# Optimization experiments

Measured on AMD Instinct MI355X. Metric: run time of the kernel, lower is better.

## Reference

```python
import jax, jax.numpy as jnp
import numpy as np

P, S, IMG = 8, 4, 256          # patch_size, stride, img_size
HID, GH, B = 64, 128, 4        # conv hidden ch, gcn hidden ch, batch
Ph = (IMG - P) // S + 1        # 63 patches per side
N = Ph * Ph                    # 3969 patch-nodes


def _conv(x, w, b):
    y = jax.lax.conv_general_dilated(x, w, (1, 1), 'SAME',
                                     dimension_numbers=('NCHW', 'OIHW', 'NCHW'))
    return y + b[None, :, None, None]


def _img2patch(x):
    # x: [B,1,H,W] -> [B, N, P*P] (row-major patch pixels, matching torch reshape)
    pt = jax.lax.conv_general_dilated_patches(x, (P, P), (S, S), 'VALID')  # [B, P*P, Ph, Pw]
    b = x.shape[0]
    return pt.reshape(b, P * P, N).transpose(0, 2, 1)


def _patch2img(y):
    # y: [b, N, P*P] -> [b, 1, IMG, IMG] via overlap scatter-add
    b = y.shape[0]
    y = y.reshape(b, Ph, Ph, P, P)
    x = jnp.zeros((b, 1, IMG, IMG), y.dtype)
    hi = S * (Ph - 1) + 1
    for i in range(P):          # fixed small loop over patch pixels (64 iters)
        for j in range(P):
            x = x.at[:, 0, i:i + hi:S, j:j + hi:S].add(y[:, :, :, i, j])
    return x


def _gcn(x, adj, w, bias):
    # x: [B,N,F_in], adj: [B,N,N] -> [B,N,F_out]
    support = jnp.einsum('bnf,fg->bng', x, w)
    return jnp.einsum('bnm,bmg->bng', adj, support) + bias


def setup_inputs() -> dict:
    key = jax.random.key(0)
    ks = jax.random.split(key, 14)
    sc = 0.05
    return {
        'input_data': jax.random.normal(ks[0], (B, 1, IMG, IMG), jnp.float32),
        'proj': jax.random.normal(ks[1], (B, 1, IMG, IMG), jnp.float32),
        'adj': jax.random.uniform(ks[2], (B, N, N), jnp.float32) / N,
        'lam': jnp.float32(0.5),
        'conv_w1': jax.random.normal(ks[3], (HID, 1, 3, 3), jnp.float32) * sc,
        'conv_b1': jnp.zeros((HID,), jnp.float32),
        'conv_w2': jax.random.normal(ks[4], (HID, HID, 3, 3), jnp.float32) * sc,
        'conv_b2': jnp.zeros((HID,), jnp.float32),
        'conv_w3': jax.random.normal(ks[5], (1, HID, 3, 3), jnp.float32) * sc,
        'conv_b3': jnp.zeros((1,), jnp.float32),
        'gcn_w3': jax.random.normal(ks[6], (P * P, GH), jnp.float32) * sc,
        'gcn_b3': jnp.zeros((GH,), jnp.float32),
        'gcn_w4': jax.random.normal(ks[7], (GH, P * P), jnp.float32) * sc,
        'gcn_b4': jnp.zeros((P * P,), jnp.float32),
    }


def reference(input_data, proj, adj, lam,
              conv_w1, conv_b1, conv_w2, conv_b2, conv_w3, conv_b3,
              gcn_w3, gcn_b3, gcn_w4, gcn_b4):
    # block1: data-fidelity step (fidelity_module modeled as DC update)
    tmp1 = input_data + lam * (proj - input_data)
    # block2: 3-layer CNN
    h = jax.nn.relu(_conv(input_data, conv_w1, conv_b1))
    h = jax.nn.relu(_conv(h, conv_w2, conv_b2))
    tmp2 = _conv(h, conv_w3, conv_b3)
    # block3/4: patch-graph GCN branch
    patch = _img2patch(input_data)                 # [B, N, P*P]
    g = jax.nn.relu(_gcn(patch, adj, gcn_w3, gcn_b3))
    g = _gcn(g, adj, gcn_w4, gcn_b4)               # [B, N, P*P]
    # Patch2Im with overlap-count normalization mask
    mask = _patch2img(jnp.ones((1, N, P * P), jnp.float32))
    tmp3 = _patch2img(g) / mask
    return jax.nn.relu(tmp1 + tmp2 + tmp3)
```

## Files before the change

### kernel.cpp

```cpp
#include <hip/hip_runtime.h>

#define IMG   256
#define NPIX  65536
#define PH    63
#define NNODE 3969
#define SN    4000
#define HID   64
#define GH    128
#define BATCH 4

typedef __attribute__((ext_vector_type(8))) short short8;
typedef __attribute__((ext_vector_type(4))) float float4v;
typedef unsigned short ushort_t;

__device__ inline ushort_t f2bf(float f) {
    union { float f; unsigned u; } v; v.f = f;
    unsigned r = v.u + 0x7FFF + ((v.u >> 16) & 1);
    return (ushort_t)(r >> 16);
}

__global__ __launch_bounds__(256) void k_cvt_adj(const float* __restrict__ adj,
                                                 ushort_t* __restrict__ adjb) {
    int n = blockIdx.x, b = blockIdx.y;
    const float* src = adj + (size_t)(b * NNODE + n) * NNODE;
    unsigned* dst = (unsigned*)(adjb + (size_t)(b * NNODE + n) * SN);
    for (int c2 = threadIdx.x; c2 < SN / 2; c2 += 256) {
        int c = c2 * 2;
        float f0 = (c < NNODE) ? src[c] : 0.f;
        float f1 = (c + 1 < NNODE) ? src[c + 1] : 0.f;
        dst[c2] = (unsigned)f2bf(f0) | ((unsigned)f2bf(f1) << 16);
    }
}

__global__ __launch_bounds__(256) void k_sup1(const float* __restrict__ in,
                                              const float* __restrict__ w3,
                                              ushort_t* __restrict__ sup1T) {
    int b = blockIdx.z;
    int g = blockIdx.y * 8 + (threadIdx.x >> 5);
    int n = blockIdx.x * 32 + (threadIdx.x & 31);
    ushort_t* dst = sup1T + (size_t)b * GH * SN + (size_t)g * SN + n;
    if (n >= NNODE) { *dst = 0; return; }
    int py = n / PH, px = n - py * PH;
    const float* base = in + (size_t)b * NPIX + (py * 4) * IMG + px * 4;
    float acc = 0.f;
#pragma unroll
    for (int i = 0; i < 8; ++i)
#pragma unroll
        for (int j = 0; j < 8; ++j)
            acc += base[i * IMG + j] * w3[(i * 8 + j) * GH + g];
    *dst = f2bf(acc);
}

template <int G>
__global__ __launch_bounds__(256) void k_gemm_mfma(const ushort_t* __restrict__ adjb,
                                                   const ushort_t* __restrict__ supT,
                                                   float* __restrict__ C) {
    constexpr int FN = (G == 128) ? 4 : 2;
    const int b = blockIdx.z, ks = blockIdx.y;
    const int node0 = blockIdx.x * 128;
    const int t = threadIdx.x;
    const int lane = t & 63, w = t >> 6;
    const int l15 = lane & 15, q = lane >> 4;
    const int wm0 = (G == 128) ? (w & 1) * 64 : 0;
    const int wn0 = (G == 128) ? (w >> 1) * 64 : w * 32;

    __shared__ ushort_t Als[G][72];
    __shared__ ushort_t Bls[128][72];

    const int k0c = ks * 992;
    const int kend = (ks == 3) ? NNODE : k0c + 992;
    const int kiters = (kend - k0c + 31) >> 5;
    const int npairs = (kiters + 1) >> 1;

    const ushort_t* Ab = supT + (size_t)b * G * SN;
    const ushort_t* Bb = adjb + (size_t)b * NNODE * SN;
    float* Cb = C + (size_t)b * G * SN;

    float4v acc[4][FN];
#pragma unroll
    for (int i = 0; i < 4; ++i)
#pragma unroll
        for (int j = 0; j < FN; ++j)
#pragma unroll
            for (int r = 0; r < 4; ++r) acc[i][j][r] = 0.f;

    for (int kp = 0; kp < npairs; ++kp) {
        const int kb0 = k0c + kp * 64;
        const bool has2 = (kp * 2 + 1 < kiters);
#pragma unroll
        for (int i = 0; i < G / 64; ++i) {
            int idx = t + i * 256;
            int r = idx >> 2, s = idx & 3;
            *(uint4*)&Als[r][s * 8] =
                *(const uint4*)&Ab[(size_t)r * SN + kb0 + s * 8];
        }
#pragma unroll
        for (int i = 0; i < 2; ++i) {
            int idx = t + i * 256;
            int r = idx >> 2, s = idx & 3;
            *(uint4*)&Bls[r][s * 8] =
                *(const uint4*)&Bb[(size_t)(node0 + r) * SN + kb0 + s * 8];
        }
        if (has2) {
#pragma unroll
            for (int i = 0; i < G / 64; ++i) {
                int idx = t + i * 256;
                int r = idx >> 2, s = idx & 3;
                *(uint4*)&Als[r][32 + s * 8] =
                    *(const uint4*)&Ab[(size_t)r * SN + kb0 + 32 + s * 8];
            }
#pragma unroll
            for (int i = 0; i < 2; ++i) {
                int idx = t + i * 256;
                int r = idx >> 2, s = idx & 3;
                *(uint4*)&Bls[r][32 + s * 8] =
                    *(const uint4*)&Bb[(size_t)(node0 + r) * SN + kb0 + 32 + s * 8];
            }
        }
        __syncthreads();
        {
            short8 af[4], bf[FN];
#pragma unroll
            for (int i = 0; i < 4; ++i)
                af[i] = *(const short8*)&Als[wm0 + i * 16 + l15][q * 8];
#pragma unroll
            for (int j = 0; j < FN; ++j)
                bf[j] = *(const short8*)&Bls[wn0 + j * 16 + l15][q * 8];
#pragma unroll
            for (int i = 0; i < 4; ++i)
#pragma unroll
                for (int j = 0; j < FN; ++j)
                    acc[i][j] = __builtin_amdgcn_mfma_f32_16x16x32_bf16(
                        af[i], bf[j], acc[i][j], 0, 0, 0);
        }
        if (has2) {
            short8 af[4], bf[FN];
#pragma unroll
            for (int i = 0; i < 4; ++i)
                af[i] = *(const short8*)&Als[wm0 + i * 16 + l15][32 + q * 8];
#pragma unroll
            for (int j = 0; j < FN; ++j)
                bf[j] = *(const short8*)&Bls[wn0 + j * 16 + l15][32 + q * 8];
#pragma unroll
            for (int i = 0; i < 4; ++i)
#pragma unroll
                for (int j = 0; j < FN; ++j)
                    acc[i][j] = __builtin_amdgcn_mfma_f32_16x16x32_bf16(
                        af[i], bf[j], acc[i][j], 0, 0, 0);
        }
        __syncthreads();
    }
#pragma unroll
    for (int i = 0; i < 4; ++i) {
        int gg = wm0 + i * 16 + q * 4;
#pragma unroll
        for (int j = 0; j < FN; ++j) {
            int nn = node0 + wn0 + j * 16 + l15;
            if (nn < NNODE) {
#pragma unroll
                for (int r = 0; r < 4; ++r)
                    unsafeAtomicAdd(&Cb[(size_t)(gg + r) * SN + nn], acc[i][j][r]);
            }
        }
    }
}

__global__ __launch_bounds__(256) void k_sup2(const float* __restrict__ g1T,
                                              const float* __restrict__ gb3,
                                              const float* __restrict__ w4,
                                              ushort_t* __restrict__ sup2T) {
    int b = blockIdx.z;
    int g = blockIdx.y * 8 + (threadIdx.x >> 5);
    int n = blockIdx.x * 32 + (threadIdx.x & 31);
    const float* gb = g1T + (size_t)b * GH * SN + n;
    float acc = 0.f;
#pragma unroll 8
    for (int k = 0; k < GH; ++k) {
        float v = fmaxf(gb[(size_t)k * SN] + gb3[k], 0.f);
        acc += v * w4[k * 64 + g];
    }
    sup2T[(size_t)b * 64 * SN + (size_t)g * SN + n] = (n < NNODE) ? f2bf(acc) : 0;
}

__global__ __launch_bounds__(256) void k_conv1(const float* __restrict__ in,
                                               const float* __restrict__ w,
                                               const float* __restrict__ bias,
                                               ushort_t* __restrict__ h1n) {
    int b = blockIdx.z;
    const float* inb = in + (size_t)b * NPIX;
    __shared__ float s[18][18];
    __shared__ float ws[576];
    int tx = threadIdx.x & 15, ty = threadIdx.x >> 4;
    int x0 = blockIdx.x * 16, y0 = blockIdx.y * 16;
    for (int idx = threadIdx.x; idx < 324; idx += 256) {
        int yy = idx / 18, xx = idx - yy * 18;
        int gy = y0 + yy - 1, gx = x0 + xx - 1;
        s[yy][xx] = (gy >= 0 && gy < IMG && gx >= 0 && gx < IMG) ? inb[gy * IMG + gx] : 0.f;
    }
    for (int idx = threadIdx.x; idx < 576; idx += 256) ws[idx] = w[idx];
    __syncthreads();
    float r[9];
#pragma unroll
    for (int dy = 0; dy < 3; ++dy)
#pragma unroll
        for (int dx = 0; dx < 3; ++dx) r[dy * 3 + dx] = s[ty + dy][tx + dx];
    int outp = (y0 + ty) * IMG + x0 + tx;
    ushort_t* dst = h1n + ((size_t)b * NPIX + outp) * 64;
#pragma unroll
    for (int sgrp = 0; sgrp < 8; ++sgrp) {
        unsigned pk[4];
#pragma unroll
        for (int h = 0; h < 4; ++h) {
            int oc0 = sgrp * 8 + h * 2;
            float a0 = bias[oc0], a1 = bias[oc0 + 1];
#pragma unroll
            for (int k = 0; k < 9; ++k) {
                a0 += r[k] * ws[oc0 * 9 + k];
                a1 += r[k] * ws[(oc0 + 1) * 9 + k];
            }
            a0 = fmaxf(a0, 0.f); a1 = fmaxf(a1, 0.f);
            pk[h] = (unsigned)f2bf(a0) | ((unsigned)f2bf(a1) << 16);
        }
        *(uint4*)&dst[sgrp * 8] = *(uint4*)pk;
    }
}

__global__ __launch_bounds__(256) void k_prepack(const float* __restrict__ w,
                                                 ushort_t* __restrict__ W2p) {
    int idx = blockIdx.x * 256 + threadIdx.x;
    if (idx >= 36864) return;
    int tap = idx >> 12, rem = idx & 4095;
    int oc = rem >> 6, ic = rem & 63;
    W2p[idx] = f2bf(w[(oc * 64 + ic) * 9 + tap]);
}

__global__ __launch_bounds__(256) void k_conv2(const ushort_t* __restrict__ h1n,
                                               const ushort_t* __restrict__ W2p,
                                               const float* __restrict__ bias,
                                               float* __restrict__ h2) {
    __shared__ ushort_t Xs[340 * 72];
    const int b = blockIdx.z;
    const ushort_t* h1b = h1n + (size_t)b * NPIX * 64;
    float* h2b = h2 + (size_t)b * 64 * NPIX;
    const int t = threadIdx.x;
    const int lane = t & 63, w = t >> 6;
    const int l15 = lane & 15, q = lane >> 4;
    const int x0 = blockIdx.x * 32, y0 = blockIdx.y * 8;

    for (int idx = t; idx < 2720; idx += 256) {
        int hp = idx >> 3, s = idx & 7;
        int hy = hp / 34, hx = hp - hy * 34;
        int gy = y0 + hy - 1, gx = x0 + hx - 1;
        uint4 v = {0u, 0u, 0u, 0u};
        if (gy >= 0 && gy < IMG && gx >= 0 && gx < IMG)
            v = *(const uint4*)&h1b[((size_t)gy * IMG + gx) * 64 + s * 8];
        *(uint4*)&Xs[hp * 72 + s * 8] = v;
    }
    __syncthreads();

    const int wn0 = w * 64;
    int pbase[4];
#pragma unroll
    for (int j = 0; j < 4; ++j) {
        int p = wn0 + j * 16 + l15;
        pbase[j] = (p >> 5) * 34 + (p & 31);
    }

    float4v acc[4][4];
#pragma unroll
    for (int i = 0; i < 4; ++i)
#pragma unroll
        for (int j = 0; j < 4; ++j)
#pragma unroll
            for (int r = 0; r < 4; ++r) acc[i][j][r] = 0.f;

    for (int tap = 0; tap < 9; ++tap) {
        int ky = tap / 3, kx = tap - ky * 3;
        const ushort_t* wp = W2p + tap * 4096;
#pragma unroll
        for (int c = 0; c < 2; ++c) {
            short8 af[4], bf[4];
#pragma unroll
            for (int i = 0; i < 4; ++i)
                af[i] = *(const short8*)&wp[(i * 16 + l15) * 64 + c * 32 + q * 8];
#pragma unroll
            for (int j = 0; j < 4; ++j)
                bf[j] = *(const short8*)&Xs[(pbase[j] + ky * 34 + kx) * 72 + c * 32 + q * 8];
#pragma unroll
            for (int i = 0; i < 4; ++i)
#pragma unroll
                for (int j = 0; j < 4; ++j)
                    acc[i][j] = __builtin_amdgcn_mfma_f32_16x16x32_bf16(
                        af[i], bf[j], acc[i][j], 0, 0, 0);
        }
    }

#pragma unroll
    for (int i = 0; i < 4; ++i) {
#pragma unroll
        for (int j = 0; j < 4; ++j) {
            int p = wn0 + j * 16 + l15;
            int y = y0 + (p >> 5), x = x0 + (p & 31);
#pragma unroll
            for (int r = 0; r < 4; ++r) {
                int oc = i * 16 + q * 4 + r;
                h2b[(size_t)oc * NPIX + (size_t)y * IMG + x] =
                    fmaxf(acc[i][j][r] + bias[oc], 0.f);
            }
        }
    }
}

__global__ __launch_bounds__(256) void k_combine(const float* __restrict__ in,
                                                 const float* __restrict__ proj,
                                                 const float* __restrict__ lamp,
                                                 const float* __restrict__ h2,
                                                 const float* __restrict__ wc,
                                                 const float* __restrict__ bc,
                                                 const float* __restrict__ g2T,
                                                 const float* __restrict__ gb4,
                                                 float* __restrict__ out) {
    int b = blockIdx.z;
    const float* inb = in + (size_t)b * NPIX;
    const float* prb = proj + (size_t)b * NPIX;
    const float* h2b = h2 + (size_t)b * 64 * NPIX;
    const float* g2b = g2T + (size_t)b * 64 * SN;
    __shared__ float s[16][18][18];
    __shared__ float ws[144];
    int tx = threadIdx.x & 15, ty = threadIdx.x >> 4;
    int x0 = blockIdx.x * 16, y0 = blockIdx.y * 16;
    int y = y0 + ty, x = x0 + tx;

    float acc = bc[0];
    for (int icc = 0; icc < 4; ++icc) {
        for (int idx = threadIdx.x; idx < 16 * 324; idx += 256) {
            int ic = idx / 324, rem = idx - ic * 324;
            int yy = rem / 18, xx = rem - yy * 18;
            int gy = y0 + yy - 1, gx = x0 + xx - 1;
            s[ic][yy][xx] = (gy >= 0 && gy < IMG && gx >= 0 && gx < IMG)
                                ? h2b[(icc * 16 + ic) * NPIX + gy * IMG + gx]
                                : 0.f;
        }
        for (int idx = threadIdx.x; idx < 144; idx += 256) ws[idx] = wc[icc * 144 + idx];
        __syncthreads();
#pragma unroll 4
        for (int ic = 0; ic < 16; ++ic) {
#pragma unroll
            for (int ky = 0; ky < 3; ++ky)
#pragma unroll
                for (int kx = 0; kx < 3; ++kx)
                    acc += s[ic][ty + ky][tx + kx] * ws[ic * 9 + ky * 3 + kx];
        }
        __syncthreads();
    }

    float iv = inb[y * IMG + x], pv = prb[y * IMG + x];
    float tmp1 = iv + lamp[0] * (pv - iv);

    int pylo = (y >= 4) ? ((y - 4) >> 2) : 0;
    int pyhi = min(62, y >> 2);
    int pxlo = (x >= 4) ? ((x - 4) >> 2) : 0;
    int pxhi = min(62, x >> 2);
    float sum = 0.f;
    int cnt = 0;
    for (int py = pylo; py <= pyhi; ++py)
        for (int px = pxlo; px <= pxhi; ++px) {
            int pix = (y - 4 * py) * 8 + (x - 4 * px);
            sum += g2b[(size_t)pix * SN + (py * PH + px)] + gb4[pix];
            ++cnt;
        }
    float tmp3 = sum / (float)cnt;

    out[(size_t)b * NPIX + y * IMG + x] = fmaxf(tmp1 + acc + tmp3, 0.f);
}

extern "C" void kernel_launch(void* const* d_in, const int* in_sizes, int n_in,
                              void* d_out, int out_size, void* d_ws, size_t ws_size,
                              hipStream_t stream) {
    const float* input = (const float*)d_in[0];
    const float* proj  = (const float*)d_in[1];
    const float* adj   = (const float*)d_in[2];
    const float* lam   = (const float*)d_in[3];
    const float* cw1   = (const float*)d_in[4];
    const float* cb1   = (const float*)d_in[5];
    const float* cw2   = (const float*)d_in[6];
    const float* cb2   = (const float*)d_in[7];
    const float* cw3   = (const float*)d_in[8];
    const float* cb3   = (const float*)d_in[9];
    const float* gw3   = (const float*)d_in[10];
    const float* gb3   = (const float*)d_in[11];
    const float* gw4   = (const float*)d_in[12];
    const float* gb4   = (const float*)d_in[13];
    float* out = (float*)d_out;

    char* base = (char*)d_ws;
    float*    g2T   = (float*)base;
    char*     pool  = base + 4096000;
    ushort_t* adjb  = (ushort_t*)pool;
    ushort_t* sup1T = (ushort_t*)(pool + 127008000);
    float*    g1T   = (float*)(pool + 127008000 + 4096000);
    ushort_t* sup2T = (ushort_t*)(pool + 127008000 + 4096000 + 8192000);
    ushort_t* h1n   = (ushort_t*)pool;
    float*    h2    = (float*)(pool + 33554432);
    ushort_t* W2p   = (ushort_t*)(pool + 33554432 + 67108864);

    dim3 blk(256);

    hipMemsetAsync(g1T, 0, 8192000, stream);
    hipMemsetAsync(g2T, 0, 4096000, stream);

    k_cvt_adj<<<dim3(NNODE, BATCH), blk, 0, stream>>>(adj, adjb);
    k_sup1<<<dim3(125, 16, BATCH), blk, 0, stream>>>(input, gw3, sup1T);
    k_gemm_mfma<128><<<dim3(32, 4, BATCH), blk, 0, stream>>>(adjb, sup1T, g1T);
    k_sup2<<<dim3(125, 8, BATCH), blk, 0, stream>>>(g1T, gb3, gw4, sup2T);
    k_gemm_mfma<64><<<dim3(32, 4, BATCH), blk, 0, stream>>>(adjb, sup2T, g2T);

    k_prepack<<<dim3(144), blk, 0, stream>>>(cw2, W2p);
    k_conv1<<<dim3(16, 16, BATCH), blk, 0, stream>>>(input, cw1, cb1, h1n);
    k_conv2<<<dim3(8, 32, BATCH), blk, 0, stream>>>(h1n, W2p, cb2, h2);
    k_combine<<<dim3(16, 16, BATCH), blk, 0, stream>>>(
        input, proj, lam, h2, cw3, cb3, g2T, gb4, out);
}
```

Measured before the change: 706.3 us.

## Fuse conv1 into conv2 tile load and fold conv3 channel reduction into conv2 epilogue

Conv1 is now recomputed per conv2 tile (including its halo) directly into shared memory, so the bf16 h1 activation tensor is never written to or read from global memory. The conv2 epilogue applies ReLU and immediately reduces the 64 channels against the conv3 weights into 9 per-tap partial maps using cross-lane shuffles. The combine kernel then only sums shifted taps from those 9 planes instead of staging 64 float channels. This removes large intermediate traffic (the 64-channel h1 and h2 tensors) in exchange for redundant conv1 work on halos and a heavier epilogue that adds register pressure.

```diff
diff --git a/kernel.cpp b/kernel.cpp
--- a/kernel.cpp
+++ b/kernel.cpp
@@ -182,49 +182,6 @@
     sup2T[(size_t)b * 64 * SN + (size_t)g * SN + n] = (n < NNODE) ? f2bf(acc) : 0;
 }
 
-__global__ __launch_bounds__(256) void k_conv1(const float* __restrict__ in,
-                                               const float* __restrict__ w,
-                                               const float* __restrict__ bias,
-                                               ushort_t* __restrict__ h1n) {
-    int b = blockIdx.z;
-    const float* inb = in + (size_t)b * NPIX;
-    __shared__ float s[18][18];
-    __shared__ float ws[576];
-    int tx = threadIdx.x & 15, ty = threadIdx.x >> 4;
-    int x0 = blockIdx.x * 16, y0 = blockIdx.y * 16;
-    for (int idx = threadIdx.x; idx < 324; idx += 256) {
-        int yy = idx / 18, xx = idx - yy * 18;
-        int gy = y0 + yy - 1, gx = x0 + xx - 1;
-        s[yy][xx] = (gy >= 0 && gy < IMG && gx >= 0 && gx < IMG) ? inb[gy * IMG + gx] : 0.f;
-    }
-    for (int idx = threadIdx.x; idx < 576; idx += 256) ws[idx] = w[idx];
-    __syncthreads();
-    float r[9];
-#pragma unroll
-    for (int dy = 0; dy < 3; ++dy)
-#pragma unroll
-        for (int dx = 0; dx < 3; ++dx) r[dy * 3 + dx] = s[ty + dy][tx + dx];
-    int outp = (y0 + ty) * IMG + x0 + tx;
-    ushort_t* dst = h1n + ((size_t)b * NPIX + outp) * 64;
-#pragma unroll
-    for (int sgrp = 0; sgrp < 8; ++sgrp) {
-        unsigned pk[4];
-#pragma unroll
-        for (int h = 0; h < 4; ++h) {
-            int oc0 = sgrp * 8 + h * 2;
-            float a0 = bias[oc0], a1 = bias[oc0 + 1];
-#pragma unroll
-            for (int k = 0; k < 9; ++k) {
-                a0 += r[k] * ws[oc0 * 9 + k];
-                a1 += r[k] * ws[(oc0 + 1) * 9 + k];
-            }
-            a0 = fmaxf(a0, 0.f); a1 = fmaxf(a1, 0.f);
-            pk[h] = (unsigned)f2bf(a0) | ((unsigned)f2bf(a1) << 16);
-        }
-        *(uint4*)&dst[sgrp * 8] = *(uint4*)pk;
-    }
-}
-
 __global__ __launch_bounds__(256) void k_prepack(const float* __restrict__ w,
                                                  ushort_t* __restrict__ W2p) {
     int idx = blockIdx.x * 256 + threadIdx.x;
@@ -234,29 +191,66 @@
     W2p[idx] = f2bf(w[(oc * 64 + ic) * 9 + tap]);
 }
 
-__global__ __launch_bounds__(256) void k_conv2(const ushort_t* __restrict__ h1n,
-                                               const ushort_t* __restrict__ W2p,
-                                               const float* __restrict__ bias,
-                                               float* __restrict__ h2) {
+__global__ __launch_bounds__(256) void k_conv2f(const float* __restrict__ in,
+                                                const float* __restrict__ w1,
+                                                const float* __restrict__ b1,
+                                                const ushort_t* __restrict__ W2p,
+                                                const float* __restrict__ b2,
+                                                const float* __restrict__ w3c,
+                                                float* __restrict__ U) {
     __shared__ ushort_t Xs[340 * 72];
+    __shared__ float pre[1088];
     const int b = blockIdx.z;
-    const ushort_t* h1b = h1n + (size_t)b * NPIX * 64;
-    float* h2b = h2 + (size_t)b * 64 * NPIX;
+    const float* inb = in + (size_t)b * NPIX;
+    float* Uball = U + (size_t)b * 9 * NPIX;
     const int t = threadIdx.x;
     const int lane = t & 63, w = t >> 6;
     const int l15 = lane & 15, q = lane >> 4;
     const int x0 = blockIdx.x * 32, y0 = blockIdx.y * 8;
 
+    float* sI  = pre;
+    float* ws1 = pre + 432;
+    float* bs1 = pre + 1008;
+
+    for (int idx = t; idx < 432; idx += 256) {
+        int yy = idx / 36, xx = idx - yy * 36;
+        int gy = y0 + yy - 2, gx = x0 + xx - 2;
+        sI[idx] = (gy >= 0 && gy < IMG && gx >= 0 && gx < IMG) ? inb[gy * IMG + gx] : 0.f;
+    }
+    for (int idx = t; idx < 576; idx += 256) ws1[idx] = w1[idx];
+    if (t < 64) bs1[t] = b1[t];
+    __syncthreads();
+
     for (int idx = t; idx < 2720; idx += 256) {
         int hp = idx >> 3, s = idx & 7;
         int hy = hp / 34, hx = hp - hy * 34;
         int gy = y0 + hy - 1, gx = x0 + hx - 1;
-        uint4 v = {0u, 0u, 0u, 0u};
-        if (gy >= 0 && gy < IMG && gx >= 0 && gx < IMG)
-            v = *(const uint4*)&h1b[((size_t)gy * IMG + gx) * 64 + s * 8];
-        *(uint4*)&Xs[hp * 72 + s * 8] = v;
+        unsigned pk[4] = {0u, 0u, 0u, 0u};
+        if (gy >= 0 && gy < IMG && gx >= 0 && gx < IMG) {
+            float r[9];
+#pragma unroll
+            for (int dy = 0; dy < 3; ++dy)
+#pragma unroll
+                for (int dx = 0; dx < 3; ++dx)
+                    r[dy * 3 + dx] = sI[(hy + dy) * 36 + hx + dx];
+#pragma unroll
+            for (int h = 0; h < 4; ++h) {
+                int oc0 = s * 8 + h * 2;
+                float a0 = bs1[oc0], a1 = bs1[oc0 + 1];
+#pragma unroll
+                for (int k = 0; k < 9; ++k) {
+                    a0 += r[k] * ws1[oc0 * 9 + k];
+                    a1 += r[k] * ws1[(oc0 + 1) * 9 + k];
+                }
+                a0 = fmaxf(a0, 0.f); a1 = fmaxf(a1, 0.f);
+                pk[h] = (unsigned)f2bf(a0) | ((unsigned)f2bf(a1) << 16);
+            }
+        }
+        *(uint4*)&Xs[hp * 72 + s * 8] = *(uint4*)pk;
     }
     __syncthreads();
+
+    for (int idx = t; idx < 576; idx += 256) pre[idx] = w3c[idx];
 
     const int wn0 = w * 64;
     int pbase[4];
@@ -294,19 +288,40 @@
                         af[i], bf[j], acc[i][j], 0, 0, 0);
         }
     }
-
-#pragma unroll
-    for (int i = 0; i < 4; ++i) {
-#pragma unroll
-        for (int j = 0; j < 4; ++j) {
-            int p = wn0 + j * 16 + l15;
-            int y = y0 + (p >> 5), x = x0 + (p & 31);
+    __syncthreads();
+
+    float b2r[16];
+#pragma unroll
+    for (int i = 0; i < 4; ++i)
+#pragma unroll
+        for (int r = 0; r < 4; ++r) b2r[i * 4 + r] = b2[i * 16 + q * 4 + r];
+
+#pragma unroll
+    for (int j = 0; j < 4; ++j) {
+        float u[9];
+#pragma unroll
+        for (int d = 0; d < 9; ++d) u[d] = 0.f;
+#pragma unroll
+        for (int i = 0; i < 4; ++i)
 #pragma unroll
             for (int r = 0; r < 4; ++r) {
                 int oc = i * 16 + q * 4 + r;
-                h2b[(size_t)oc * NPIX + (size_t)y * IMG + x] =
-                    fmaxf(acc[i][j][r] + bias[oc], 0.f);
+                float h = fmaxf(acc[i][j][r] + b2r[i * 4 + r], 0.f);
+#pragma unroll
+                for (int d = 0; d < 9; ++d) u[d] += h * pre[oc * 9 + d];
             }
+#pragma unroll
+        for (int d = 0; d < 9; ++d) {
+            u[d] += __shfl_xor(u[d], 16, 64);
+            u[d] += __shfl_xor(u[d], 32, 64);
+        }
+        int p = wn0 + j * 16 + l15;
+        int y = y0 + (p >> 5), x = x0 + (p & 31);
+#pragma unroll
+        for (int dd = 0; dd < 3; ++dd) {
+            int d = q + dd * 4;
+            if (d < 9)
+                Uball[(size_t)d * NPIX + (size_t)y * IMG + x] = u[d];
         }
     }
 }
@@ -314,8 +329,7 @@
 __global__ __launch_bounds__(256) void k_combine(const float* __restrict__ in,
                                                  const float* __restrict__ proj,
                                                  const float* __restrict__ lamp,
-                                                 const float* __restrict__ h2,
-                                                 const float* __restrict__ wc,
+                                                 const float* __restrict__ U,
                                                  const float* __restrict__ bc,
                                                  const float* __restrict__ g2T,
                                                  const float* __restrict__ gb4,
@@ -323,35 +337,21 @@
     int b = blockIdx.z;
     const float* inb = in + (size_t)b * NPIX;
     const float* prb = proj + (size_t)b * NPIX;
-    const float* h2b = h2 + (size_t)b * 64 * NPIX;
+    const float* Ub = U + (size_t)b * 9 * NPIX;
     const float* g2b = g2T + (size_t)b * 64 * SN;
-    __shared__ float s[16][18][18];
-    __shared__ float ws[144];
     int tx = threadIdx.x & 15, ty = threadIdx.x >> 4;
-    int x0 = blockIdx.x * 16, y0 = blockIdx.y * 16;
-    int y = y0 + ty, x = x0 + tx;
+    int x = blockIdx.x * 16 + tx, y = blockIdx.y * 16 + ty;
 
     float acc = bc[0];
-    for (int icc = 0; icc < 4; ++icc) {
-        for (int idx = threadIdx.x; idx < 16 * 324; idx += 256) {
-            int ic = idx / 324, rem = idx - ic * 324;
-            int yy = rem / 18, xx = rem - yy * 18;
-            int gy = y0 + yy - 1, gx = x0 + xx - 1;
-            s[ic][yy][xx] = (gy >= 0 && gy < IMG && gx >= 0 && gx < IMG)
-                                ? h2b[(icc * 16 + ic) * NPIX + gy * IMG + gx]
-                                : 0.f;
-        }
-        for (int idx = threadIdx.x; idx < 144; idx += 256) ws[idx] = wc[icc * 144 + idx];
-        __syncthreads();
-#pragma unroll 4
-        for (int ic = 0; ic < 16; ++ic) {
-#pragma unroll
-            for (int ky = 0; ky < 3; ++ky)
-#pragma unroll
-                for (int kx = 0; kx < 3; ++kx)
-                    acc += s[ic][ty + ky][tx + kx] * ws[ic * 9 + ky * 3 + kx];
-        }
-        __syncthreads();
+#pragma unroll
+    for (int dy = 0; dy < 3; ++dy) {
+        int yy = y + dy - 1;
+#pragma unroll
+        for (int dx = 0; dx < 3; ++dx) {
+            int xx = x + dx - 1;
+            if (yy >= 0 && yy < IMG && xx >= 0 && xx < IMG)
+                acc += Ub[(size_t)(dy * 3 + dx) * NPIX + (size_t)yy * IMG + xx];
+        }
     }
 
     float iv = inb[y * IMG + x], pv = prb[y * IMG + x];
@@ -400,9 +400,8 @@
     ushort_t* sup1T = (ushort_t*)(pool + 127008000);
     float*    g1T   = (float*)(pool + 127008000 + 4096000);
     ushort_t* sup2T = (ushort_t*)(pool + 127008000 + 4096000 + 8192000);
-    ushort_t* h1n   = (ushort_t*)pool;
-    float*    h2    = (float*)(pool + 33554432);
-    ushort_t* W2p   = (ushort_t*)(pool + 33554432 + 67108864);
+    float*    U     = (float*)pool;
+    ushort_t* W2p   = (ushort_t*)(pool + 9437184);
 
     dim3 blk(256);
 
@@ -416,8 +415,7 @@
     k_gemm_mfma<64><<<dim3(32, 4, BATCH), blk, 0, stream>>>(adjb, sup2T, g2T);
 
     k_prepack<<<dim3(144), blk, 0, stream>>>(cw2, W2p);
-    k_conv1<<<dim3(16, 16, BATCH), blk, 0, stream>>>(input, cw1, cb1, h1n);
-    k_conv2<<<dim3(8, 32, BATCH), blk, 0, stream>>>(h1n, W2p, cb2, h2);
+    k_conv2f<<<dim3(8, 32, BATCH), blk, 0, stream>>>(input, cw1, cb1, W2p, cb2, cw3, U);
     k_combine<<<dim3(16, 16, BATCH), blk, 0, stream>>>(
-        input, proj, lam, h2, cw3, cb3, g2T, gb4, out);
-}
+        input, proj, lam, U, cb3, g2T, gb4, out);
+}
```

Result: faster. 669.0 us (-5.3%).
